# Optimization experiments

Measured on AMD Instinct MI355X. Metric: run time of the kernel, lower is better.

Reference implementation:

```python
import jax, jax.numpy as jnp
import numpy as np

EPS = 1e-08

def setup_inputs() -> dict:
    key = jax.random.key(0)
    ks = jax.random.split(key, 7)
    B, O, A, D, H = 64, 100, 16, 1024, 512
    return {
        "obj_vecs_i": jax.random.normal(ks[0], (B, O, D), dtype=jnp.float32),
        "attr_feats": jax.random.normal(ks[1], (B, O, A, D), dtype=jnp.float32),
        "p_attr_feats": jax.random.normal(ks[2], (B, O, A, H), dtype=jnp.float32),
        "attr_masks": jax.random.randint(ks[3], (B, O, A), 0, 2, dtype=jnp.int32),
        "W_obj": jax.random.normal(ks[4], (H, D), dtype=jnp.float32) * 0.02,
        "b_obj": jax.random.normal(ks[5], (H,), dtype=jnp.float32) * 0.02,
        "w_alpha": jax.random.normal(ks[6], (H,), dtype=jnp.float32) * 0.02,
        "b_alpha": jnp.zeros((), dtype=jnp.float32),
    }

def reference(obj_vecs_i, attr_feats, p_attr_feats, attr_masks, W_obj, b_obj, w_alpha, b_alpha):
    # obj2att: [B,O,D] -> [B,O,H]
    att_obj = jnp.einsum('bod,hd->boh', obj_vecs_i, W_obj) + b_obj
    # additive score: tanh(p + q) then project to scalar per attribute
    dot = jnp.tanh(p_attr_feats + att_obj[:, :, None, :])          # [B,O,A,H]
    scores = jnp.einsum('boah,h->boa', dot, w_alpha) + b_alpha     # [B,O,A]
    weight = jax.nn.softmax(scores, axis=-1)                       # [B,O,A]
    # masked renormalization
    weight = weight * attr_masks.astype(weight.dtype)
    weight = weight / (jnp.sum(weight, axis=-1, keepdims=True) + EPS)
    # weighted-sum pooling over attributes
    att_res = jnp.einsum('boa,boad->bod', weight, attr_feats)      # [B,O,D]
    return att_res
```

## Files before the change

### kernel.cpp

```cpp
#include <hip/hip_runtime.h>
#include <stdint.h>

#define EPS 1e-8f

typedef __attribute__((ext_vector_type(8))) __bf16 bf16x8;
typedef __attribute__((ext_vector_type(4))) float f32x4;

static constexpr int BO = 6400;
static constexpr int AA = 16;
static constexpr int DD = 1024;
static constexpr int HH = 512;

__device__ __forceinline__ unsigned short f2bf(float x) {
    uint32_t b = __float_as_uint(x);
    b += 0x7fffu + ((b >> 16) & 1u);
    return (unsigned short)(b >> 16);
}

__device__ __forceinline__ float fast_tanh(float x) {
    float e = __expf(2.0f * x);
    return 1.0f - __fdividef(2.0f, e + 1.0f);
}

__global__ __launch_bounds__(256) void k_prep_w(const float* __restrict__ W,
                                                unsigned short* __restrict__ W_bf) {
    const int i = blockIdx.x * 256 + threadIdx.x;
    const long off = (long)i * 8;
    float4 v0 = *(const float4*)(W + off);
    float4 v1 = *(const float4*)(W + off + 4);
    union { unsigned short u[8]; int4 v; } pk;
    pk.u[0] = f2bf(v0.x); pk.u[1] = f2bf(v0.y); pk.u[2] = f2bf(v0.z); pk.u[3] = f2bf(v0.w);
    pk.u[4] = f2bf(v1.x); pk.u[5] = f2bf(v1.y); pk.u[6] = f2bf(v1.z); pk.u[7] = f2bf(v1.w);
    *(int4*)(W_bf + off) = pk.v;
}

__global__ __launch_bounds__(64) void k_gemm(const float* __restrict__ obj,
                                             const unsigned short* __restrict__ W_bf,
                                             const float* __restrict__ b_obj,
                                             float* __restrict__ att_obj) {
    const int lane = threadIdx.x;
    const int xcd  = blockIdx.x & 7;
    const int j    = blockIdx.x >> 3;
    const int mt   = xcd * 13 + (j % 13);
    if (mt >= 100) return;
    const int nt   = j / 13;
    const int m0   = mt * 64;
    const int n0   = nt * 64;
    const int lr   = lane & 15;
    const int lk   = (lane >> 4) * 8;

    const float*          ap = obj  + (size_t)(m0 + lr) * DD + lk;
    const unsigned short* bp = W_bf + (size_t)(n0 + lr) * DD + lk;

    f32x4 acc[4][4];
    #pragma unroll
    for (int i = 0; i < 4; ++i)
        #pragma unroll
        for (int jj = 0; jj < 4; ++jj) acc[i][jj] = f32x4{0.f, 0.f, 0.f, 0.f};

    float4 a_lo[4], a_hi[4];
    bf16x8 bfr[4];
    #pragma unroll
    for (int i = 0; i < 4; ++i) {
        a_lo[i] = *(const float4*)(ap + (size_t)i * 16 * DD);
        a_hi[i] = *(const float4*)(ap + (size_t)i * 16 * DD + 4);
        bfr[i]  = *(const bf16x8*)(bp + (size_t)i * 16 * DD);
    }

    #pragma unroll 1
    for (int k0 = 0; k0 < DD; k0 += 32) {
        const int kn = (k0 + 32 < DD) ? (k0 + 32) : 0;
        float4 na_lo[4], na_hi[4];
        bf16x8 nb[4];
        #pragma unroll
        for (int i = 0; i < 4; ++i) {
            na_lo[i] = *(const float4*)(ap + (size_t)i * 16 * DD + kn);
            na_hi[i] = *(const float4*)(ap + (size_t)i * 16 * DD + kn + 4);
            nb[i]    = *(const bf16x8*)(bp + (size_t)i * 16 * DD + kn);
        }
        bf16x8 afr[4];
        #pragma unroll
        for (int i = 0; i < 4; ++i) {
            afr[i][0] = (__bf16)a_lo[i].x; afr[i][1] = (__bf16)a_lo[i].y;
            afr[i][2] = (__bf16)a_lo[i].z; afr[i][3] = (__bf16)a_lo[i].w;
            afr[i][4] = (__bf16)a_hi[i].x; afr[i][5] = (__bf16)a_hi[i].y;
            afr[i][6] = (__bf16)a_hi[i].z; afr[i][7] = (__bf16)a_hi[i].w;
        }
        #pragma unroll
        for (int i = 0; i < 4; ++i)
            #pragma unroll
            for (int jj = 0; jj < 4; ++jj)
                acc[i][jj] = __builtin_amdgcn_mfma_f32_16x16x32_bf16(afr[i], bfr[jj], acc[i][jj], 0, 0, 0);
        #pragma unroll
        for (int i = 0; i < 4; ++i) { a_lo[i] = na_lo[i]; a_hi[i] = na_hi[i]; bfr[i] = nb[i]; }
    }

    const int crow = (lane >> 4) * 4;
    #pragma unroll
    for (int jj = 0; jj < 4; ++jj) {
        const int n = n0 + jj * 16 + lr;
        const float bb = b_obj[n];
        #pragma unroll
        for (int i = 0; i < 4; ++i) {
            #pragma unroll
            for (int r = 0; r < 4; ++r)
                att_obj[(size_t)(m0 + i * 16 + crow + r) * HH + n] = acc[i][jj][r] + bb;
        }
    }
}

__global__ __launch_bounds__(256, 5) void k_attn(const float* __restrict__ att_obj,
                                                 const float* __restrict__ p_attr,
                                                 const int* __restrict__ masks,
                                                 const float* __restrict__ w_alpha,
                                                 const float* __restrict__ attr_feats,
                                                 float* __restrict__ out) {
    const int wv   = threadIdx.x >> 6;
    const int lane = threadIdx.x & 63;
    const int row  = blockIdx.x * 4 + wv;

    int mbits;
    {
        const int4* m4 = (const int4*)(masks + (size_t)row * AA);
        int4 a = m4[0], b = m4[1], c = m4[2], d = m4[3];
        mbits =  (a.x)      | (a.y << 1)  | (a.z << 2)  | (a.w << 3)
              | (b.x << 4) | (b.y << 5)  | (b.z << 6)  | (b.w << 7)
              | (c.x << 8) | (c.y << 9)  | (c.z << 10) | (c.w << 11)
              | (d.x << 12)| (d.y << 13) | (d.z << 14) | (d.w << 15);
    }

    const float* prow = p_attr     + (size_t)row * AA * HH;
    const float* arow = attr_feats + (size_t)row * AA * DD;

    float sc[AA];
    {
        const f32x4* att4 = (const f32x4*)(att_obj + (size_t)row * HH);
        const f32x4* wa4  = (const f32x4*)w_alpha;
        const f32x4 av0 = att4[lane], av1 = att4[64 + lane];
        const f32x4 wv0 = wa4[lane],  wv1 = wa4[64 + lane];

        #pragma unroll 2
        for (int a = 0; a < AA; ++a) {
            if (mbits >> a & 1) {
                const f32x4* pa = (const f32x4*)(prow + (size_t)a * HH);
                f32x4 x0 = pa[lane];
                f32x4 x1 = pa[64 + lane];
                float s;
                s  = wv0.x * fast_tanh(x0.x + av0.x);
                s += wv0.y * fast_tanh(x0.y + av0.y);
                s += wv0.z * fast_tanh(x0.z + av0.z);
                s += wv0.w * fast_tanh(x0.w + av0.w);
                s += wv1.x * fast_tanh(x1.x + av1.x);
                s += wv1.y * fast_tanh(x1.y + av1.y);
                s += wv1.z * fast_tanh(x1.z + av1.z);
                s += wv1.w * fast_tanh(x1.w + av1.w);
                sc[a] = s;
            } else {
                sc[a] = 0.f;
            }
        }
    }

    #pragma unroll
    for (int d = 1; d < 64; d <<= 1) {
        #pragma unroll
        for (int a = 0; a < AA; ++a) sc[a] += __shfl_xor(sc[a], d);
    }

    float mx = -3.0e38f;
    #pragma unroll
    for (int a = 0; a < AA; ++a)
        if (mbits >> a & 1) mx = fmaxf(mx, sc[a]);
    float T = 0.f;
    #pragma unroll
    for (int a = 0; a < AA; ++a) {
        float e = (mbits >> a & 1) ? __expf(sc[a] - mx) : 0.f;
        sc[a] = e;
        T += e;
    }
    const float inv = (T > 0.f) ? 1.0f / (T * (1.0f + EPS)) : 0.f;
    #pragma unroll
    for (int a = 0; a < AA; ++a) sc[a] *= inv;

    f32x4 acc0 = {0.f,0.f,0.f,0.f}, acc1 = acc0, acc2 = acc0, acc3 = acc0;
    #pragma unroll 2
    for (int a = 0; a < AA; ++a) {
        if (mbits >> a & 1) {
            const f32x4* a4 = (const f32x4*)(arow + (size_t)a * DD);
            f32x4 v0 = a4[       lane];
            f32x4 v1 = a4[ 64 + lane];
            f32x4 v2 = a4[128 + lane];
            f32x4 v3 = a4[192 + lane];
            const float w = sc[a];
            acc0 += w * v0;
            acc1 += w * v1;
            acc2 += w * v2;
            acc3 += w * v3;
        }
    }
    f32x4* o4 = (f32x4*)(out + (size_t)row * DD);
    o4[      lane] = acc0;
    o4[ 64 + lane] = acc1;
    o4[128 + lane] = acc2;
    o4[192 + lane] = acc3;
}

extern "C" void kernel_launch(void* const* d_in, const int* in_sizes, int n_in,
                              void* d_out, int out_size, void* d_ws, size_t ws_size,
                              hipStream_t stream) {
    const float* obj_vecs   = (const float*)d_in[0];
    const float* attr_feats = (const float*)d_in[1];
    const float* p_attr     = (const float*)d_in[2];
    const int*   masks      = (const int*)d_in[3];
    const float* W_obj      = (const float*)d_in[4];
    const float* b_obj      = (const float*)d_in[5];
    const float* w_alpha    = (const float*)d_in[6];
    float* out = (float*)d_out;

    char* ws = (char*)d_ws;
    float*          att_obj = (float*)ws;
    unsigned short* W_bf    = (unsigned short*)(ws + 13107200);

    k_prep_w<<<256, 256, 0, stream>>>(W_obj, W_bf);
    k_gemm<<<832, 64, 0, stream>>>(obj_vecs, W_bf, b_obj, att_obj);
    k_attn<<<BO / 4, 256, 0, stream>>>(att_obj, p_attr, masks, w_alpha, attr_feats, out);
}
```

Measured before the change: 130.2 us.

## Map one row per block, splitting attributes across waves with shared-memory scores

The attention kernel now gives each 256-thread block one (b,o) row instead of four. Each wave scores four attributes and reduces each with its own shuffle chain, and the scores are exchanged through shared memory behind a barrier. The pooling loop then has every thread cover four output elements, with eight attribute loads batched before accumulation to raise memory-level parallelism. This adds a __syncthreads and four times as many blocks, and each block repeats the small softmax in every thread.

```diff
diff --git a/kernel.cpp b/kernel.cpp
--- a/kernel.cpp
+++ b/kernel.cpp
@@ -115,9 +115,12 @@
                                                  const float* __restrict__ w_alpha,
                                                  const float* __restrict__ attr_feats,
                                                  float* __restrict__ out) {
-    const int wv   = threadIdx.x >> 6;
-    const int lane = threadIdx.x & 63;
-    const int row  = blockIdx.x * 4 + wv;
+    __shared__ float s_sc[AA];
+
+    const int tid  = threadIdx.x;
+    const int wv   = tid >> 6;
+    const int lane = tid & 63;
+    const int row  = blockIdx.x;
 
     int mbits;
     {
@@ -132,77 +135,82 @@
     const float* prow = p_attr     + (size_t)row * AA * HH;
     const float* arow = attr_feats + (size_t)row * AA * DD;
 
-    float sc[AA];
     {
         const f32x4* att4 = (const f32x4*)(att_obj + (size_t)row * HH);
         const f32x4* wa4  = (const f32x4*)w_alpha;
         const f32x4 av0 = att4[lane], av1 = att4[64 + lane];
         const f32x4 wv0 = wa4[lane],  wv1 = wa4[64 + lane];
 
-        #pragma unroll 2
-        for (int a = 0; a < AA; ++a) {
+        f32x4 x0[4], x1[4];
+        #pragma unroll
+        for (int q = 0; q < 4; ++q) {
+            const int a = wv * 4 + q;
             if (mbits >> a & 1) {
                 const f32x4* pa = (const f32x4*)(prow + (size_t)a * HH);
-                f32x4 x0 = pa[lane];
-                f32x4 x1 = pa[64 + lane];
+                x0[q] = pa[lane];
+                x1[q] = pa[64 + lane];
+            }
+        }
+        #pragma unroll
+        for (int q = 0; q < 4; ++q) {
+            const int a = wv * 4 + q;
+            if (mbits >> a & 1) {
                 float s;
-                s  = wv0.x * fast_tanh(x0.x + av0.x);
-                s += wv0.y * fast_tanh(x0.y + av0.y);
-                s += wv0.z * fast_tanh(x0.z + av0.z);
-                s += wv0.w * fast_tanh(x0.w + av0.w);
-                s += wv1.x * fast_tanh(x1.x + av1.x);
-                s += wv1.y * fast_tanh(x1.y + av1.y);
-                s += wv1.z * fast_tanh(x1.z + av1.z);
-                s += wv1.w * fast_tanh(x1.w + av1.w);
-                sc[a] = s;
-            } else {
-                sc[a] = 0.f;
+                s  = wv0.x * fast_tanh(x0[q].x + av0.x);
+                s += wv0.y * fast_tanh(x0[q].y + av0.y);
+                s += wv0.z * fast_tanh(x0[q].z + av0.z);
+                s += wv0.w * fast_tanh(x0[q].w + av0.w);
+                s += wv1.x * fast_tanh(x1[q].x + av1.x);
+                s += wv1.y * fast_tanh(x1[q].y + av1.y);
+                s += wv1.z * fast_tanh(x1[q].z + av1.z);
+                s += wv1.w * fast_tanh(x1[q].w + av1.w);
+                s += __shfl_xor(s, 1);
+                s += __shfl_xor(s, 2);
+                s += __shfl_xor(s, 4);
+                s += __shfl_xor(s, 8);
+                s += __shfl_xor(s, 16);
+                s += __shfl_xor(s, 32);
+                if (lane == 0) s_sc[a] = s;
             }
         }
     }
-
-    #pragma unroll
-    for (int d = 1; d < 64; d <<= 1) {
-        #pragma unroll
-        for (int a = 0; a < AA; ++a) sc[a] += __shfl_xor(sc[a], d);
-    }
-
-    float mx = -3.0e38f;
-    #pragma unroll
-    for (int a = 0; a < AA; ++a)
-        if (mbits >> a & 1) mx = fmaxf(mx, sc[a]);
-    float T = 0.f;
-    #pragma unroll
-    for (int a = 0; a < AA; ++a) {
-        float e = (mbits >> a & 1) ? __expf(sc[a] - mx) : 0.f;
-        sc[a] = e;
-        T += e;
-    }
-    const float inv = (T > 0.f) ? 1.0f / (T * (1.0f + EPS)) : 0.f;
-    #pragma unroll
-    for (int a = 0; a < AA; ++a) sc[a] *= inv;
-
-    f32x4 acc0 = {0.f,0.f,0.f,0.f}, acc1 = acc0, acc2 = acc0, acc3 = acc0;
-    #pragma unroll 2
-    for (int a = 0; a < AA; ++a) {
-        if (mbits >> a & 1) {
-            const f32x4* a4 = (const f32x4*)(arow + (size_t)a * DD);
-            f32x4 v0 = a4[       lane];
-            f32x4 v1 = a4[ 64 + lane];
-            f32x4 v2 = a4[128 + lane];
-            f32x4 v3 = a4[192 + lane];
-            const float w = sc[a];
-            acc0 += w * v0;
-            acc1 += w * v1;
-            acc2 += w * v2;
-            acc3 += w * v3;
-        }
-    }
-    f32x4* o4 = (f32x4*)(out + (size_t)row * DD);
-    o4[      lane] = acc0;
-    o4[ 64 + lane] = acc1;
-    o4[128 + lane] = acc2;
-    o4[192 + lane] = acc3;
+    __syncthreads();
+
+    float w[AA];
+    {
+        float mx = -3.0e38f;
+        #pragma unroll
+        for (int a = 0; a < AA; ++a)
+            mx = fmaxf(mx, (mbits >> a & 1) ? s_sc[a] : -3.0e38f);
+        float T = 0.f;
+        #pragma unroll
+        for (int a = 0; a < AA; ++a) {
+            float e = (mbits >> a & 1) ? __expf(s_sc[a] - mx) : 0.f;
+            w[a] = e;
+            T += e;
+        }
+        const float inv = (T > 0.f) ? 1.0f / (T * (1.0f + EPS)) : 0.f;
+        #pragma unroll
+        for (int a = 0; a < AA; ++a) w[a] *= inv;
+    }
+
+    const f32x4* af4 = (const f32x4*)arow;
+    f32x4 acc = {0.f, 0.f, 0.f, 0.f};
+    #pragma unroll
+    for (int h = 0; h < 2; ++h) {
+        f32x4 v[8];
+        #pragma unroll
+        for (int q = 0; q < 8; ++q) {
+            const int a = h * 8 + q;
+            if (mbits >> a & 1) v[q] = af4[a * 256 + tid];
+        }
+        #pragma unroll
+        for (int q = 0; q < 8; ++q) {
+            const int a = h * 8 + q;
+            if (mbits >> a & 1) acc += w[a] * v[q];
+        }
+    }
+    *(f32x4*)(out + (size_t)row * DD + tid * 4) = acc;
 }
 
 extern "C" void kernel_launch(void* const* d_in, const int* in_sizes, int n_in,
@@ -223,5 +231,5 @@
 
     k_prep_w<<<256, 256, 0, stream>>>(W_obj, W_bf);
     k_gemm<<<832, 64, 0, stream>>>(obj_vecs, W_bf, b_obj, att_obj);
-    k_attn<<<BO / 4, 256, 0, stream>>>(att_obj, p_attr, masks, w_alpha, attr_feats, out);
-}
+    k_attn<<<BO, 256, 0, stream>>>(att_obj, p_attr, masks, w_alpha, attr_feats, out);
+}
```

Result: faster. 121.9 us (-6.4%).
